# Optimization experiments

Measured on AMD Instinct MI355X. Metric: run time of the kernel, lower is better.

## Reference

```python
import jax, jax.numpy as jnp
import numpy as np

VOCAB = 100000
EMBED = 128
MAX_STORY_LEN = 50
HOPS = 3


def setup_inputs() -> dict:
    key = jax.random.key(0)
    k1, k2, k3, k4, k5 = jax.random.split(key, 5)
    x = jax.random.randint(k1, (64, 50, 64), 0, VOCAB)
    q = jax.random.randint(k2, (64, 16), 0, VOCAB)
    # (hops+1) embedding tables, N(0, 0.1), row 0 zeroed (padding idx convention)
    A = jax.random.normal(k3, (HOPS + 1, VOCAB, EMBED), dtype=jnp.float32) * 0.1
    A = A.at[:, 0, :].set(0.0)
    TA = jax.random.normal(k4, (1, MAX_STORY_LEN + 1, EMBED), dtype=jnp.float32) * 0.1
    TC = jax.random.normal(k5, (1, MAX_STORY_LEN + 1, EMBED), dtype=jnp.float32) * 0.1
    return {"x": x, "q": q, "A": A, "TA": TA, "TC": TC}


def _position_encoding(J, d):
    # l_kj = 1 - j/J - (k/d) * (1 - 2j/J), 1-indexed j,k
    j = jnp.arange(1, J + 1, dtype=jnp.float32)[:, None] / J   # [J,1]
    k = jnp.arange(1, d + 1, dtype=jnp.float32)[None, :] / d   # [1,d]
    return 1.0 - j - k * (1.0 - 2.0 * j)                        # [J,d]


def reference(x, q, A, TA, TC):
    bs, story_len, s_sent_len = x.shape
    d = A.shape[-1]
    hops = A.shape[0] - 1
    pe = _position_encoding(s_sent_len, d)            # [J,d], broadcasts over [bs,story,J,d]
    ta = TA[:, :story_len, :]                          # [1,story,d]
    tc = TC[:, :story_len, :]
    # dropout inactive (eval / p folded to identity)
    u = A[0][q].sum(axis=1)                            # B = A[0]; [bs,d]
    for h in range(hops):
        m = (A[h][x] * pe).sum(axis=2) + ta            # gather+PE scale+sum-pool+TE: [bs,story,d]
        c = A[h + 1][x].sum(axis=2) + tc               # [bs,story,d]
        p = jax.nn.softmax(jnp.einsum('bsd,bd->bs', m, u), axis=-1)
        u = jnp.einsum('bs,bsd->bd', p, c) + u
    out = u @ A[-1].T                                  # W = A[-1].weight^T: [bs,vocab]
    return jax.nn.log_softmax(out, axis=-1)
```

## Files before the change

kernel.cpp:

```cpp
#include <hip/hip_runtime.h>
#include <hip/hip_bf16.h>

#define BS 64
#define SL 50
#define SW 64
#define DIM 128
#define VOC 100000
#define VT 6250
#define K4_BLOCKS 1563

typedef __attribute__((ext_vector_type(8))) short short8;
typedef __attribute__((ext_vector_type(4))) float float4v;

__device__ __forceinline__ short f2b(float f){
    unsigned int u = __float_as_uint(f);
    u += 0x7fffu + ((u >> 16) & 1u);
    return (short)(u >> 16);
}

__global__ __launch_bounds__(256) void k_gather(const int* __restrict__ x,
    const float* __restrict__ A, const float* __restrict__ TA,
    const float* __restrict__ TC, float* __restrict__ m, float* __restrict__ c)
{
    int s = blockIdx.x, b = blockIdx.y;
    int tid = threadIdx.x;
    int wv = tid >> 6, l = tid & 63;
    const int* xp = x + (b * SL + s) * SW;
    const float2* A2 = (const float2*)A;
    float aPE[3][2] = {{0.f,0.f},{0.f,0.f},{0.f,0.f}};
    float aPL[3][2] = {{0.f,0.f},{0.f,0.f},{0.f,0.f}};
    float kk0 = (2*l + 1) * (1.0f / DIM);
    float kk1 = (2*l + 2) * (1.0f / DIM);
    for (int wi = 0; wi < 16; ++wi) {
        int word = wv * 16 + wi;
        int idx  = xp[word];
        float j    = (word + 1) * (1.0f / SW);
        float om   = 1.0f - 2.0f * j;
        float base = 1.0f - j;
        float pe0 = base - kk0 * om, pe1 = base - kk1 * om;
        size_t roff = (size_t)idx * 64 + l;
        #pragma unroll
        for (int t = 0; t < 4; ++t) {
            float2 v = A2[(size_t)t * VOC * 64 + roff];
            if (t < 3) { aPE[t][0] += v.x * pe0; aPE[t][1] += v.y * pe1; }
            if (t > 0) { aPL[t-1][0] += v.x;     aPL[t-1][1] += v.y;     }
        }
    }
    __shared__ float red[4][6][DIM];
    #pragma unroll
    for (int t = 0; t < 3; ++t) {
        red[wv][t  ][2*l] = aPE[t][0]; red[wv][t  ][2*l+1] = aPE[t][1];
        red[wv][3+t][2*l] = aPL[t][0]; red[wv][3+t][2*l+1] = aPL[t][1];
    }
    __syncthreads();
    if (tid < DIM) {
        int d = tid;
        float ta = TA[s * DIM + d];
        float tc = TC[s * DIM + d];
        #pragma unroll
        for (int t = 0; t < 3; ++t) {
            float spe = red[0][t][d] + red[1][t][d] + red[2][t][d] + red[3][t][d];
            float spl = red[0][3+t][d] + red[1][3+t][d] + red[2][3+t][d] + red[3][3+t][d];
            size_t o = (((size_t)t * BS + b) * SL + s) * DIM + d;
            m[o] = spe + ta;
            c[o] = spl + tc;
        }
    }
}

__global__ void k_query(const int* __restrict__ q, const float* __restrict__ A,
                        float* __restrict__ u)
{
    int b = blockIdx.x, l = threadIdx.x;
    const float2* A2 = (const float2*)A;
    float a0 = 0.f, a1 = 0.f;
    for (int t = 0; t < 16; ++t) {
        int idx = q[b * 16 + t];
        float2 v = A2[(size_t)idx * 64 + l];
        a0 += v.x; a1 += v.y;
    }
    u[b * DIM + 2*l]     = a0;
    u[b * DIM + 2*l + 1] = a1;
}

__global__ void k_hop(const float* __restrict__ mh, const float* __restrict__ ch,
                      float* __restrict__ u)
{
    int b = blockIdx.x, l = threadIdx.x;
    float u0 = u[b * DIM + 2*l], u1 = u[b * DIM + 2*l + 1];
    __shared__ float sc[SL];
    const float2* mb = (const float2*)(mh + (size_t)b * SL * DIM);
    for (int s = 0; s < SL; ++s) {
        float2 w = mb[s * 64 + l];
        float p = w.x * u0 + w.y * u1;
        for (int off = 32; off; off >>= 1) p += __shfl_down(p, off);
        if (l == 0) sc[s] = p;
    }
    __syncthreads();
    float mx = -1e30f;
    for (int s = 0; s < SL; ++s) mx = fmaxf(mx, sc[s]);
    float sum = 0.f;
    for (int s = 0; s < SL; ++s) sum += __expf(sc[s] - mx);
    float inv = 1.0f / sum;
    const float2* cb = (const float2*)(ch + (size_t)b * SL * DIM);
    float a0 = u0, a1 = u1;
    for (int s = 0; s < SL; ++s) {
        float p = __expf(sc[s] - mx) * inv;
        float2 w = cb[s * 64 + l];
        a0 += p * w.x;
        a1 += p * w.y;
    }
    u[b * DIM + 2*l]     = a0;
    u[b * DIM + 2*l + 1] = a1;
}

__global__ void k_cast(const float* __restrict__ u, short* __restrict__ u16)
{
    int i = blockIdx.x * 256 + threadIdx.x;
    if (i < BS * DIM) u16[i] = f2b(u[i]);
}

__global__ __launch_bounds__(256) void k_logits(const float* __restrict__ A3,
    const short* __restrict__ u16, float* __restrict__ out)
{
    int tid = threadIdx.x;
    int wv = tid >> 6, lane = tid & 63;
    int n = lane & 15, qd = lane >> 4;
    int tile = blockIdx.x * 4 + wv;
    if (tile >= VT) return;
    short8 bfr[4];
    size_t brow = ((size_t)(tile * 16 + n)) * DIM + qd * 8;
    #pragma unroll
    for (int k = 0; k < 4; ++k) {
        const float* p = A3 + brow + (size_t)k * 32;
        float4v f0 = *(const float4v*)p;
        float4v f1 = *(const float4v*)(p + 4);
        bfr[k] = (short8){ f2b(f0.x), f2b(f0.y), f2b(f0.z), f2b(f0.w),
                           f2b(f1.x), f2b(f1.y), f2b(f1.z), f2b(f1.w) };
    }
    float4v acc[4];
    #pragma unroll
    for (int bt = 0; bt < 4; ++bt) {
        acc[bt] = (float4v){0.f, 0.f, 0.f, 0.f};
        size_t arow = ((size_t)(bt * 16 + n)) * DIM + qd * 8;
        #pragma unroll
        for (int k = 0; k < 4; ++k) {
            short8 af = *(const short8*)(u16 + arow + (size_t)k * 32);
            acc[bt] = __builtin_amdgcn_mfma_f32_16x16x32_bf16(af, bfr[k], acc[bt], 0, 0, 0);
        }
    }
    int v = tile * 16 + n;
    #pragma unroll
    for (int bt = 0; bt < 4; ++bt) {
        #pragma unroll
        for (int r = 0; r < 4; ++r) {
            int b = bt * 16 + qd * 4 + r;
            out[(size_t)b * VOC + v] = acc[bt][r];
        }
    }
}

__global__ void k_lsepart(const float* __restrict__ out, float* __restrict__ part)
{
    int j = blockIdx.x, b = blockIdx.y;
    int tid = threadIdx.x;
    const float4v* row = (const float4v*)(out + (size_t)b * VOC);
    float s = 0.f;
    int lo = j * 3125, hi = lo + 3125;
    for (int i = lo + tid; i < hi; i += 256) {
        float4v v = row[i];
        s += __expf(v.x) + __expf(v.y) + __expf(v.z) + __expf(v.w);
    }
    __shared__ float red[256];
    red[tid] = s;
    __syncthreads();
    for (int off = 128; off; off >>= 1) {
        if (tid < off) red[tid] += red[tid + off];
        __syncthreads();
    }
    if (tid == 0) part[b * 8 + j] = red[0];
}

__global__ void k_sub(float* __restrict__ out, const float* __restrict__ part)
{
    int b = blockIdx.y;
    int i = blockIdx.x * 256 + threadIdx.x;
    float s = 0.f;
    #pragma unroll
    for (int j = 0; j < 8; ++j) s += part[b * 8 + j];
    float l = logf(s);
    if (i < VOC / 4) {
        float4v* p = (float4v*)(out + (size_t)b * VOC) + i;
        float4v t = *p;
        t.x -= l; t.y -= l; t.z -= l; t.w -= l;
        *p = t;
    }
}

extern "C" void kernel_launch(void* const* d_in, const int* in_sizes, int n_in,
                              void* d_out, int out_size, void* d_ws, size_t ws_size,
                              hipStream_t stream)
{
    const int*   x  = (const int*)d_in[0];
    const int*   q  = (const int*)d_in[1];
    const float* A  = (const float*)d_in[2];
    const float* TA = (const float*)d_in[3];
    const float* TC = (const float*)d_in[4];
    float* out = (float*)d_out;

    char*  ws   = (char*)d_ws;
    float* u    = (float*)ws;
    short* u16  = (short*)(ws + 32768);
    float* part = (float*)(ws + 49152);

    float* m = out;
    float* c = m + (size_t)3 * BS * SL * DIM;

    k_gather<<<dim3(SL, BS), 256, 0, stream>>>(x, A, TA, TC, m, c);
    k_query<<<BS, 64, 0, stream>>>(q, A, u);
    for (int h = 0; h < 3; ++h)
        k_hop<<<BS, 64, 0, stream>>>(m + (size_t)h * BS * SL * DIM,
                                     c + (size_t)h * BS * SL * DIM, u);
    k_cast<<<(BS * DIM + 255) / 256, 256, 0, stream>>>(u, u16);
    k_logits<<<K4_BLOCKS, 256, 0, stream>>>(A + (size_t)3 * VOC * DIM, u16, out);
    k_lsepart<<<dim3(8, BS), 256, 0, stream>>>(out, part);
    k_sub<<<dim3((VOC / 4 + 255) / 256, BS), 256, 0, stream>>>(out, part);
}
```

Measured before the change: 427.2 us.

## Fuse query and hops kernels, fold exp-sum into logits GEMM, stage u in LDS

Merges the query embedding, three hop kernels and the bf16 cast into a single per-batch kernel, removing several launches. The logits kernel now stages the bf16 query vectors in shared memory and computes per-block partial exp-sums as it stores logits, so the separate pass that re-reads the 25.6 MB logits matrix is dropped and replaced by a small reduction over partials. The gather kernel loads all word indices once per wave and broadcasts them with shuffles, and its loop is unrolled. The cost is a larger partial-sum buffer and extra shuffle reductions in the GEMM epilogue.

```diff
diff --git a/kernel.cpp b/kernel.cpp
--- a/kernel.cpp
+++ b/kernel.cpp
@@ -26,14 +26,16 @@
     int tid = threadIdx.x;
     int wv = tid >> 6, l = tid & 63;
     const int* xp = x + (b * SL + s) * SW;
+    int myidx = xp[l];
     const float2* A2 = (const float2*)A;
     float aPE[3][2] = {{0.f,0.f},{0.f,0.f},{0.f,0.f}};
     float aPL[3][2] = {{0.f,0.f},{0.f,0.f},{0.f,0.f}};
     float kk0 = (2*l + 1) * (1.0f / DIM);
     float kk1 = (2*l + 2) * (1.0f / DIM);
+    #pragma unroll
     for (int wi = 0; wi < 16; ++wi) {
         int word = wv * 16 + wi;
-        int idx  = xp[word];
+        int idx  = __shfl(myidx, word);
         float j    = (word + 1) * (1.0f / SW);
         float om   = 1.0f - 2.0f * j;
         float base = 1.0f - j;
@@ -68,109 +70,113 @@
     }
 }
 
-__global__ void k_query(const int* __restrict__ q, const float* __restrict__ A,
-                        float* __restrict__ u)
+__global__ void k_hops(const int* __restrict__ q, const float* __restrict__ A,
+                       const float* __restrict__ m, const float* __restrict__ c,
+                       short* __restrict__ u16)
 {
     int b = blockIdx.x, l = threadIdx.x;
     const float2* A2 = (const float2*)A;
-    float a0 = 0.f, a1 = 0.f;
+    float u0 = 0.f, u1 = 0.f;
     for (int t = 0; t < 16; ++t) {
         int idx = q[b * 16 + t];
         float2 v = A2[(size_t)idx * 64 + l];
-        a0 += v.x; a1 += v.y;
-    }
-    u[b * DIM + 2*l]     = a0;
-    u[b * DIM + 2*l + 1] = a1;
-}
-
-__global__ void k_hop(const float* __restrict__ mh, const float* __restrict__ ch,
-                      float* __restrict__ u)
-{
-    int b = blockIdx.x, l = threadIdx.x;
-    float u0 = u[b * DIM + 2*l], u1 = u[b * DIM + 2*l + 1];
+        u0 += v.x; u1 += v.y;
+    }
     __shared__ float sc[SL];
-    const float2* mb = (const float2*)(mh + (size_t)b * SL * DIM);
-    for (int s = 0; s < SL; ++s) {
-        float2 w = mb[s * 64 + l];
-        float p = w.x * u0 + w.y * u1;
-        for (int off = 32; off; off >>= 1) p += __shfl_down(p, off);
-        if (l == 0) sc[s] = p;
-    }
-    __syncthreads();
-    float mx = -1e30f;
-    for (int s = 0; s < SL; ++s) mx = fmaxf(mx, sc[s]);
-    float sum = 0.f;
-    for (int s = 0; s < SL; ++s) sum += __expf(sc[s] - mx);
-    float inv = 1.0f / sum;
-    const float2* cb = (const float2*)(ch + (size_t)b * SL * DIM);
-    float a0 = u0, a1 = u1;
-    for (int s = 0; s < SL; ++s) {
-        float p = __expf(sc[s] - mx) * inv;
-        float2 w = cb[s * 64 + l];
-        a0 += p * w.x;
-        a1 += p * w.y;
-    }
-    u[b * DIM + 2*l]     = a0;
-    u[b * DIM + 2*l + 1] = a1;
-}
-
-__global__ void k_cast(const float* __restrict__ u, short* __restrict__ u16)
-{
-    int i = blockIdx.x * 256 + threadIdx.x;
-    if (i < BS * DIM) u16[i] = f2b(u[i]);
+    for (int h = 0; h < 3; ++h) {
+        const float2* mb = (const float2*)(m + ((size_t)h * BS + b) * SL * DIM);
+        const float2* cb = (const float2*)(c + ((size_t)h * BS + b) * SL * DIM);
+        for (int s = 0; s < SL; ++s) {
+            float2 w = mb[s * 64 + l];
+            float p = w.x * u0 + w.y * u1;
+            for (int off = 32; off; off >>= 1) p += __shfl_down(p, off);
+            if (l == 0) sc[s] = p;
+        }
+        __syncthreads();
+        float mx = -1e30f;
+        for (int s = 0; s < SL; ++s) mx = fmaxf(mx, sc[s]);
+        float sum = 0.f;
+        for (int s = 0; s < SL; ++s) sum += __expf(sc[s] - mx);
+        float inv = 1.0f / sum;
+        float a0 = u0, a1 = u1;
+        for (int s = 0; s < SL; ++s) {
+            float p = __expf(sc[s] - mx) * inv;
+            float2 w = cb[s * 64 + l];
+            a0 += p * w.x;
+            a1 += p * w.y;
+        }
+        u0 = a0; u1 = a1;
+        __syncthreads();
+    }
+    u16[b * DIM + 2*l]     = f2b(u0);
+    u16[b * DIM + 2*l + 1] = f2b(u1);
 }
 
 __global__ __launch_bounds__(256) void k_logits(const float* __restrict__ A3,
-    const short* __restrict__ u16, float* __restrict__ out)
-{
+    const short* __restrict__ u16g, float* __restrict__ out, float* __restrict__ part)
+{
+    __shared__ short su[BS * DIM];
+    __shared__ float lpart[4][64];
     int tid = threadIdx.x;
+    const int* ug = (const int*)u16g;
+    int* us = (int*)su;
+    #pragma unroll
+    for (int i = 0; i < 16; ++i) us[tid + 256 * i] = ug[tid + 256 * i];
     int wv = tid >> 6, lane = tid & 63;
+    lpart[wv][lane] = 0.0f;
+    __syncthreads();
     int n = lane & 15, qd = lane >> 4;
     int tile = blockIdx.x * 4 + wv;
-    if (tile >= VT) return;
-    short8 bfr[4];
-    size_t brow = ((size_t)(tile * 16 + n)) * DIM + qd * 8;
-    #pragma unroll
-    for (int k = 0; k < 4; ++k) {
-        const float* p = A3 + brow + (size_t)k * 32;
-        float4v f0 = *(const float4v*)p;
-        float4v f1 = *(const float4v*)(p + 4);
-        bfr[k] = (short8){ f2b(f0.x), f2b(f0.y), f2b(f0.z), f2b(f0.w),
-                           f2b(f1.x), f2b(f1.y), f2b(f1.z), f2b(f1.w) };
-    }
-    float4v acc[4];
-    #pragma unroll
-    for (int bt = 0; bt < 4; ++bt) {
-        acc[bt] = (float4v){0.f, 0.f, 0.f, 0.f};
-        size_t arow = ((size_t)(bt * 16 + n)) * DIM + qd * 8;
+    if (tile < VT) {
+        short8 bfr[4];
+        size_t brow = ((size_t)(tile * 16 + n)) * DIM + qd * 8;
         #pragma unroll
         for (int k = 0; k < 4; ++k) {
-            short8 af = *(const short8*)(u16 + arow + (size_t)k * 32);
-            acc[bt] = __builtin_amdgcn_mfma_f32_16x16x32_bf16(af, bfr[k], acc[bt], 0, 0, 0);
-        }
-    }
-    int v = tile * 16 + n;
-    #pragma unroll
-    for (int bt = 0; bt < 4; ++bt) {
-        #pragma unroll
-        for (int r = 0; r < 4; ++r) {
-            int b = bt * 16 + qd * 4 + r;
-            out[(size_t)b * VOC + v] = acc[bt][r];
-        }
-    }
-}
-
-__global__ void k_lsepart(const float* __restrict__ out, float* __restrict__ part)
-{
-    int j = blockIdx.x, b = blockIdx.y;
-    int tid = threadIdx.x;
-    const float4v* row = (const float4v*)(out + (size_t)b * VOC);
+            const float* p = A3 + brow + (size_t)k * 32;
+            float4v f0 = *(const float4v*)p;
+            float4v f1 = *(const float4v*)(p + 4);
+            bfr[k] = (short8){ f2b(f0.x), f2b(f0.y), f2b(f0.z), f2b(f0.w),
+                               f2b(f1.x), f2b(f1.y), f2b(f1.z), f2b(f1.w) };
+        }
+        float4v acc[4];
+        #pragma unroll
+        for (int bt = 0; bt < 4; ++bt) {
+            acc[bt] = (float4v){0.f, 0.f, 0.f, 0.f};
+            int arow = (bt * 16 + n) * DIM + qd * 8;
+            #pragma unroll
+            for (int k = 0; k < 4; ++k) {
+                short8 af = *(const short8*)(su + arow + k * 32);
+                acc[bt] = __builtin_amdgcn_mfma_f32_16x16x32_bf16(af, bfr[k], acc[bt], 0, 0, 0);
+            }
+        }
+        int v = tile * 16 + n;
+        #pragma unroll
+        for (int bt = 0; bt < 4; ++bt) {
+            #pragma unroll
+            for (int r = 0; r < 4; ++r) {
+                int b = bt * 16 + qd * 4 + r;
+                float val = acc[bt][r];
+                out[(size_t)b * VOC + v] = val;
+                float e = __expf(val);
+                e += __shfl_xor(e, 1);
+                e += __shfl_xor(e, 2);
+                e += __shfl_xor(e, 4);
+                e += __shfl_xor(e, 8);
+                if (n == 0) lpart[wv][b] = e;
+            }
+        }
+    }
+    __syncthreads();
+    if (tid < 64)
+        part[(size_t)blockIdx.x * 64 + tid] =
+            lpart[0][tid] + lpart[1][tid] + lpart[2][tid] + lpart[3][tid];
+}
+
+__global__ void k_lse(const float* __restrict__ part, float* __restrict__ lse)
+{
+    int b = blockIdx.x, tid = threadIdx.x;
     float s = 0.f;
-    int lo = j * 3125, hi = lo + 3125;
-    for (int i = lo + tid; i < hi; i += 256) {
-        float4v v = row[i];
-        s += __expf(v.x) + __expf(v.y) + __expf(v.z) + __expf(v.w);
-    }
+    for (int i = tid; i < K4_BLOCKS; i += 256) s += part[(size_t)i * 64 + b];
     __shared__ float red[256];
     red[tid] = s;
     __syncthreads();
@@ -178,17 +184,14 @@
         if (tid < off) red[tid] += red[tid + off];
         __syncthreads();
     }
-    if (tid == 0) part[b * 8 + j] = red[0];
-}
-
-__global__ void k_sub(float* __restrict__ out, const float* __restrict__ part)
+    if (tid == 0) lse[b] = logf(red[0]);
+}
+
+__global__ void k_sub(float* __restrict__ out, const float* __restrict__ lse)
 {
     int b = blockIdx.y;
     int i = blockIdx.x * 256 + threadIdx.x;
-    float s = 0.f;
-    #pragma unroll
-    for (int j = 0; j < 8; ++j) s += part[b * 8 + j];
-    float l = logf(s);
+    float l = lse[b];
     if (i < VOC / 4) {
         float4v* p = (float4v*)(out + (size_t)b * VOC) + i;
         float4v t = *p;
@@ -209,20 +212,16 @@
     float* out = (float*)d_out;
 
     char*  ws   = (char*)d_ws;
-    float* u    = (float*)ws;
-    short* u16  = (short*)(ws + 32768);
-    float* part = (float*)(ws + 49152);
+    short* u16  = (short*)ws;
+    float* part = (float*)(ws + 16384);
+    float* lse  = (float*)(ws + 16384 + 400128);
 
     float* m = out;
     float* c = m + (size_t)3 * BS * SL * DIM;
 
     k_gather<<<dim3(SL, BS), 256, 0, stream>>>(x, A, TA, TC, m, c);
-    k_query<<<BS, 64, 0, stream>>>(q, A, u);
-    for (int h = 0; h < 3; ++h)
-        k_hop<<<BS, 64, 0, stream>>>(m + (size_t)h * BS * SL * DIM,
-                                     c + (size_t)h * BS * SL * DIM, u);
-    k_cast<<<(BS * DIM + 255) / 256, 256, 0, stream>>>(u, u16);
-    k_logits<<<K4_BLOCKS, 256, 0, stream>>>(A + (size_t)3 * VOC * DIM, u16, out);
-    k_lsepart<<<dim3(8, BS), 256, 0, stream>>>(out, part);
-    k_sub<<<dim3((VOC / 4 + 255) / 256, BS), 256, 0, stream>>>(out, part);
-}
+    k_hops<<<BS, 64, 0, stream>>>(q, A, m, c, u16);
+    k_logits<<<K4_BLOCKS, 256, 0, stream>>>(A + (size_t)3 * VOC * DIM, u16, out, part);
+    k_lse<<<BS, 256, 0, stream>>>(part, lse);
+    k_sub<<<dim3((VOC / 4 + 255) / 256, BS), 256, 0, stream>>>(out, lse);
+}
```

New measurement: 408.9 us. -4.3%, faster.
